# Kernel tuning notes

Measured on AMD Instinct MI355X. Metric: run time of the kernel, lower is better.

The kernel has to match this reference:

```python
import jax, jax.numpy as jnp
import numpy as np

KERNEL_SIZE = 11  # int(resolution / 11.6) with resolution=128
SIGMA = 1.5
K1, K2 = 0.01, 0.03


def gaussian_kernel(k=KERNEL_SIZE, sigma=SIGMA):
    coords = jnp.arange(k, dtype=jnp.float32) - (k - 1) / 2
    g = jnp.exp(-coords ** 2 / (2 * sigma ** 2))
    g = g / g.sum()
    return jnp.outer(g, g)  # (k,k)


def depthwise_conv(x, kern):
    # x: (N,C,H,W), kern: (k,k); depthwise (groups=C), SAME padding, stride 1
    C = x.shape[1]
    k = kern.shape[0]
    w = jnp.broadcast_to(kern[None, None], (C, 1, k, k))
    return jax.lax.conv_general_dilated(
        x, w, window_strides=(1, 1), padding='SAME',
        feature_group_count=C,
        dimension_numbers=('NCHW', 'OIHW', 'NCHW'))


def dssim_map(x, y, kern):
    C1, C2 = K1 ** 2, K2 ** 2
    mu_x = depthwise_conv(x, kern)
    mu_y = depthwise_conv(y, kern)
    sigma_x = depthwise_conv(x * x, kern) - mu_x ** 2
    sigma_y = depthwise_conv(y * y, kern) - mu_y ** 2
    sigma_xy = depthwise_conv(x * y, kern) - mu_x * mu_y
    ssim_num = (2 * mu_x * mu_y + C1) * (2 * sigma_xy + C2)
    ssim_den = (mu_x ** 2 + mu_y ** 2 + C1) * (sigma_x + sigma_y + C2)
    ssim = ssim_num / (ssim_den + 1e-8)
    return (1 - ssim) / 2  # (N,C,H,W)


def poly_mask(pts, H, W):
    # pts: (P,2) polygon vertices (x, y). Vectorized ray-casting point-in-polygon,
    # restricted to the truncated bounding box exactly like the torch code
    # (mask[:, :, ymin:ymax, xmin:xmax] slice), and zeroed if polygon exits frame.
    x, y = pts[:, 0], pts[:, 1]
    xmin, xmax = jnp.floor(x.min()), jnp.floor(x.max())  # == int() for positive coords
    ymin, ymax = jnp.floor(y.min()), jnp.floor(y.max())
    valid = (xmin >= 0) & (ymin >= 0) & (xmax < W) & (ymax < H)
    yy, xx = jnp.meshgrid(jnp.arange(H, dtype=jnp.float32),
                          jnp.arange(W, dtype=jnp.float32), indexing='ij')
    x1, y1 = x[:, None, None], y[:, None, None]        # (P,1,1)
    x2 = jnp.roll(x, -1)[:, None, None]
    y2 = jnp.roll(y, -1)[:, None, None]
    Y, X = yy[None], xx[None]                          # (1,H,W)
    cond = ((y1 > Y) != (y2 > Y)) & (X < (x2 - x1) * (Y - y1) / (y2 - y1 + 1e-6) + x1)
    inside = (cond.sum(axis=0) % 2) == 1               # XOR-fold over edges, (H,W)
    bbox = (yy >= ymin) & (yy < ymax) & (xx >= xmin) & (xx < xmax)
    return jnp.where(valid, (inside & bbox).astype(jnp.float32), 0.0)


def weight_map(lmrk, H, W):
    # lmrk: (68,2). weight = 1 + 3*eyeL + 3*eyeR + 2*mouth (additive, as in torch)
    return (1.0
            + 3.0 * poly_mask(lmrk[36:42], H, W)
            + 3.0 * poly_mask(lmrk[42:48], H, W)
            + 2.0 * poly_mask(lmrk[48:60], H, W))  # (H,W)


def setup_inputs() -> dict:
    key = jax.random.key(0)
    k1, k2, k3 = jax.random.split(key, 3)
    N, C, H, W = 48, 3, 256, 256
    pred = jax.random.normal(k1, (N, C, H, W), dtype=jnp.float32)
    target = jax.random.normal(k2, (N, C, H, W), dtype=jnp.float32)
    # landmarks strictly inside the frame so all polygons are rasterized
    landmarks = 20.0 + 216.0 * jax.random.uniform(k3, (N, 68, 2), dtype=jnp.float32)
    return {"pred": pred, "target": target, "landmarks": landmarks}


def reference(pred, target, landmarks):
    N, C, H, W = pred.shape
    kern = gaussian_kernel()
    # per-sample DSSIM (batch-of-1 conv in torch == batched conv here)
    d = dssim_map(pred, target, kern).mean(axis=(1, 2, 3))          # (N,)
    abs_diff = jnp.abs(pred - target)
    l1 = abs_diff.mean(axis=(1, 2, 3))                              # (N,)
    wmap = jax.vmap(lambda lm: weight_map(lm, H, W))(landmarks)     # (N,H,W)
    lw = (wmap[:, None] * abs_diff).mean(axis=(1, 2, 3))            # (N,)
    return (10.0 * d + 10.0 * l1 + 5.0 * lw).mean()
```

## Files before the change

### kernel.cpp

```cpp
#include <hip/hip_runtime.h>
#include <cmath>

#define HW 256
#define NIMG 48
#define NCH 3
#define NPLANE (NIMG * NCH)
#define STRIP 37
#define NSTRIP 7
#define NIN (STRIP + 10)
#define CHUNK 22
#define NCHUNK 3
#define NSLOT 64

__global__ void zero_ws_kernel(double* ws) {
    if (threadIdx.x < NSLOT) ws[threadIdx.x] = 0.0;
}

__launch_bounds__(256)
__global__ void fused_kernel(const float* __restrict__ pred,
                             const float* __restrict__ target,
                             const float* __restrict__ lmk,
                             double* __restrict__ ws)
{
    const int plane = blockIdx.x;
    const int n     = plane / 3;
    const int r0    = blockIdx.y * STRIP;
    const int x     = threadIdx.x;

    __shared__ float4 mva[2][HW + 10];
    __shared__ float  mvb[2][HW + 10];
    __shared__ float  sxc[STRIP][24];
    __shared__ int    srowflag[STRIP];
    __shared__ float  slm[48];
    __shared__ float  sbbs[12];
    __shared__ float  svalids[3];
    __shared__ float  red[12];

    float g6[6];
    {
        float gg[11]; float gs = 0.f;
#pragma unroll
        for (int q = 0; q < 11; ++q) {
            float c = (float)q - 5.0f;
            gg[q] = expf(-c * c / 4.5f);
            gs += gg[q];
        }
#pragma unroll
        for (int q = 0; q < 6; ++q) g6[q] = gg[q] / gs;
    }
#define GW(j) g6[(j) < 6 ? (j) : 10 - (j)]

    if (x < 48) slm[x] = lmk[n * 136 + 72 + x];
    if (x < 5) {
        const float4 z4 = make_float4(0.f, 0.f, 0.f, 0.f);
        mva[0][x] = z4; mva[0][261 + x] = z4;
        mva[1][x] = z4; mva[1][261 + x] = z4;
        mvb[0][x] = 0.f; mvb[0][261 + x] = 0.f;
        mvb[1][x] = 0.f; mvb[1][261 + x] = 0.f;
    }
    __syncthreads();

    if (x < 3) {
        const int s0 = (x == 0) ? 0 : (x == 1) ? 6 : 12;
        const int L  = (x == 2) ? 12 : 6;
        float xmn = 3e38f, xmx = -3e38f, ymn = 3e38f, ymx = -3e38f;
        for (int q = 0; q < L; ++q) {
            float px = slm[2 * (s0 + q)], py = slm[2 * (s0 + q) + 1];
            xmn = fminf(xmn, px); xmx = fmaxf(xmx, px);
            ymn = fminf(ymn, py); ymx = fmaxf(ymx, py);
        }
        xmn = floorf(xmn); xmx = floorf(xmx); ymn = floorf(ymn); ymx = floorf(ymx);
        sbbs[4 * x + 0] = xmn; sbbs[4 * x + 1] = xmx;
        sbbs[4 * x + 2] = ymn; sbbs[4 * x + 3] = ymx;
        svalids[x] = (xmn >= 0.f && ymn >= 0.f && xmx < 256.f && ymx < 256.f) ? 1.f : 0.f;
    }

#pragma unroll
    for (int u = 0; u < (STRIP * 24 + 255) / 256; ++u) {
        int idx = x + 256 * u;
        if (idx < STRIP * 24) {
            int r = idx / 24, e = idx - r * 24;
            float Y = (float)(r0 + r);
            const int s0 = (e < 6) ? 0 : (e < 12) ? 6 : 12;
            const int L  = (e < 12) ? 6 : 12;
            int il = e - s0;
            int i2 = (il + 1 == L) ? 0 : il + 1;
            float x1 = slm[2 * (s0 + il)], y1 = slm[2 * (s0 + il) + 1];
            float x2 = slm[2 * (s0 + i2)], y2 = slm[2 * (s0 + i2) + 1];
            bool crossing = (y1 > Y) != (y2 > Y);
            float xc = (x2 - x1) * (Y - y1) / (y2 - y1 + 1e-6f) + x1;
            sxc[r][e] = crossing ? xc : -3e38f;
        }
    }
    __syncthreads();

    if (x < STRIP) {
        float Y = (float)(r0 + x);
        int f = 0;
        if (svalids[0] != 0.f && Y >= sbbs[2]  && Y < sbbs[3])  f |= 1;
        if (svalids[1] != 0.f && Y >= sbbs[6]  && Y < sbbs[7])  f |= 2;
        if (svalids[2] != 0.f && Y >= sbbs[10] && Y < sbbs[11]) f |= 4;
        srowflag[x] = f;
    }
    __syncthreads();

    const float* __restrict__ pp = pred   + (size_t)plane * (HW * HW) + x;
    const float* __restrict__ tp = target + (size_t)plane * (HW * HW) + x;

    float rp[11], rt[11];
    float pfap, pfat, pfbp, pfbt;
    {
        int ra = r0 - 5;
        bool va = (ra >= 0);
        pfap = va ? pp[(size_t)ra * HW] : 0.f;
        pfat = va ? tp[(size_t)ra * HW] : 0.f;
        int rb = r0 - 4;
        bool vb = (rb >= 0);
        pfbp = vb ? pp[(size_t)rb * HW] : 0.f;
        pfbt = vb ? tp[(size_t)rb * HW] : 0.f;
    }

    float acc = 0.f, accl1 = 0.f, acclw = 0.f;
    const float X = (float)x;

    for (int c = 0; c < NCHUNK; ++c) {
#pragma unroll
        for (int t = 0; t < CHUNK; ++t) {
            const int i  = CHUNK * c + t;
            const int sr = t % 11;

            if (i < NIN) {
                if ((t & 1) == 0) { rp[sr] = pfap; rt[sr] = pfat; }
                else              { rp[sr] = pfbp; rt[sr] = pfbt; }
                {
                    int rin2 = r0 - 3 + i;
                    bool v = (i + 2 < NIN) && (rin2 >= 0) && (rin2 < HW);
                    float lp = 0.f, lt = 0.f;
                    if (v) {
                        lp = pp[(size_t)rin2 * HW];
                        lt = tp[(size_t)rin2 * HW];
                    }
                    if ((t & 1) == 0) { pfap = lp; pfat = lt; }
                    else              { pfbp = lp; pfbt = lt; }
                }

                if (i >= 5 && i < 5 + STRIP) {
                    int r_in = r0 - 5 + i;
                    if (r_in < HW) {
                        float ad = fabsf(rp[sr] - rt[sr]);
                        accl1 += ad;
                        float wgt = 1.f;
                        const int flags = srowflag[i - 5];
                        if (flags) {
                            const float* xc = sxc[i - 5];
                            int c0 = 0, c1 = 0, c2 = 0;
#pragma unroll
                            for (int e = 0; e < 6; ++e)   c0 += (X < xc[e]) ? 1 : 0;
#pragma unroll
                            for (int e = 6; e < 12; ++e)  c1 += (X < xc[e]) ? 1 : 0;
#pragma unroll
                            for (int e = 12; e < 24; ++e) c2 += (X < xc[e]) ? 1 : 0;
                            if ((flags & 1) && (c0 & 1) && X >= sbbs[0] && X < sbbs[1]) wgt += 3.f;
                            if ((flags & 2) && (c1 & 1) && X >= sbbs[4] && X < sbbs[5]) wgt += 3.f;
                            if ((flags & 4) && (c2 & 1) && X >= sbbs[8] && X < sbbs[9]) wgt += 2.f;
                        }
                        acclw += wgt * ad;
                    }
                }
            }

            if (i >= 10 && i < 10 + STRIP) {
                int r = r0 + i - 10;
                if (r < HW) {
                    float mux = 0.f, muy = 0.f, exx = 0.f, eyy = 0.f, exy = 0.f;
#pragma unroll
                    for (int j = 0; j < 11; ++j) {
                        const int s = (t + 1 + j) % 11;
                        float w = GW(j);
                        float p = rp[s], q = rt[s];
                        float wp = w * p, wt = w * q;
                        mux += wp; muy += wt;
                        exx = fmaf(wp, p, exx);
                        eyy = fmaf(wt, q, eyy);
                        exy = fmaf(wp, q, exy);
                    }
                    mva[t & 1][x + 5] = make_float4(mux, muy, exx, eyy);
                    mvb[t & 1][x + 5] = exy;
                }
            }

            if (i >= 11 && i < 11 + STRIP) {
                int rr = r0 + i - 11;
                if (rr < HW) {
                    const int b = (t + 1) & 1;
                    float Mx = 0.f, My = 0.f, Exx = 0.f, Eyy = 0.f, Exy = 0.f;
#pragma unroll
                    for (int k = 0; k < 11; ++k) {
                        float w = GW(k);
                        float4 m4 = mva[b][x + k];
                        float  m1 = mvb[b][x + k];
                        Mx  = fmaf(w, m4.x, Mx);
                        My  = fmaf(w, m4.y, My);
                        Exx = fmaf(w, m4.z, Exx);
                        Eyy = fmaf(w, m4.w, Eyy);
                        Exy = fmaf(w, m1,  Exy);
                    }
                    float sx  = Exx - Mx * Mx;
                    float sy  = Eyy - My * My;
                    float sxy = Exy - Mx * My;
                    const float C1 = 1e-4f, C2 = 9e-4f;
                    float num = (2.f * Mx * My + C1) * (2.f * sxy + C2);
                    float den = (Mx * Mx + My * My + C1) * (sx + sy + C2);
                    acc += 0.5f * (1.f - num / (den + 1e-8f));
                }
            }

            asm volatile("s_waitcnt lgkmcnt(0)" ::: "memory");
            __builtin_amdgcn_s_barrier();
        }
    }

#pragma unroll
    for (int off = 32; off > 0; off >>= 1) {
        acc   += __shfl_down(acc, off, 64);
        accl1 += __shfl_down(accl1, off, 64);
        acclw += __shfl_down(acclw, off, 64);
    }
    if ((x & 63) == 0) {
        int w = x >> 6;
        red[w] = acc; red[4 + w] = accl1; red[8 + w] = acclw;
    }
    __syncthreads();
    if (x == 0) {
        double s = 10.0 * ((double)red[0] + red[1] + red[2]  + red[3])
                 + 10.0 * ((double)red[4] + red[5] + red[6]  + red[7])
                 +  5.0 * ((double)red[8] + red[9] + red[10] + red[11]);
        atomicAdd(&ws[(blockIdx.y * NPLANE + blockIdx.x) & (NSLOT - 1)], s);
    }
}

__global__ void final_kernel(const double* __restrict__ ws, float* __restrict__ out) {
    double v = ws[threadIdx.x];
#pragma unroll
    for (int off = 32; off > 0; off >>= 1)
        v += __shfl_down(v, off, 64);
    if (threadIdx.x == 0) {
        const double denom = (double)NIMG * NCH * HW * HW;
        out[0] = (float)(v / denom);
    }
}

extern "C" void kernel_launch(void* const* d_in, const int* in_sizes, int n_in,
                              void* d_out, int out_size, void* d_ws, size_t ws_size,
                              hipStream_t stream)
{
    const float* pred   = (const float*)d_in[0];
    const float* target = (const float*)d_in[1];
    const float* lmk    = (const float*)d_in[2];
    float* out  = (float*)d_out;
    double* ws  = (double*)d_ws;

    hipLaunchKernelGGL(zero_ws_kernel, dim3(1), dim3(64), 0, stream, ws);
    hipLaunchKernelGGL(fused_kernel, dim3(NPLANE, NSTRIP), dim3(256), 0, stream,
                       pred, target, lmk, ws);
    hipLaunchKernelGGL(final_kernel, dim3(1), dim3(64), 0, stream, ws, out);
}
```

Measured before the change: 153.0 us.

## Process two rows per barrier phase with double-buffered pairs of vertical sums

Restructures the row-streaming loop so each barrier-separated phase handles two input rows. Vertical convolution results go into paired, double-buffered shared-memory slots, and the horizontal pass reads the previous phase's pair. This roughly halves the number of workgroup barriers per strip and gives more independent work between them. The cost is doubled LDS for the intermediate buffers, a one-row-longer pipeline delay for the horizontal stage, and possibly higher register pressure.

```diff
diff --git a/kernel.cpp b/kernel.cpp
--- a/kernel.cpp
+++ b/kernel.cpp
@@ -8,8 +8,8 @@
 #define STRIP 37
 #define NSTRIP 7
 #define NIN (STRIP + 10)
-#define CHUNK 22
 #define NCHUNK 3
+#define PHASES 25
 #define NSLOT 64
 
 __global__ void zero_ws_kernel(double* ws) {
@@ -27,8 +27,8 @@
     const int r0    = blockIdx.y * STRIP;
     const int x     = threadIdx.x;
 
-    __shared__ float4 mva[2][HW + 10];
-    __shared__ float  mvb[2][HW + 10];
+    __shared__ float4 mva[2][2][HW + 10];
+    __shared__ float  mvb[2][2][HW + 10];
     __shared__ float  sxc[STRIP][24];
     __shared__ int    srowflag[STRIP];
     __shared__ float  slm[48];
@@ -53,10 +53,13 @@
     if (x < 48) slm[x] = lmk[n * 136 + 72 + x];
     if (x < 5) {
         const float4 z4 = make_float4(0.f, 0.f, 0.f, 0.f);
-        mva[0][x] = z4; mva[0][261 + x] = z4;
-        mva[1][x] = z4; mva[1][261 + x] = z4;
-        mvb[0][x] = 0.f; mvb[0][261 + x] = 0.f;
-        mvb[1][x] = 0.f; mvb[1][261 + x] = 0.f;
+#pragma unroll
+        for (int b = 0; b < 2; ++b)
+#pragma unroll
+            for (int q = 0; q < 2; ++q) {
+                mva[b][q][x] = z4; mva[b][q][261 + x] = z4;
+                mvb[b][q][x] = 0.f; mvb[b][q][261 + x] = 0.f;
+            }
     }
     __syncthreads();
 
@@ -125,93 +128,109 @@
 
     for (int c = 0; c < NCHUNK; ++c) {
 #pragma unroll
-        for (int t = 0; t < CHUNK; ++t) {
-            const int i  = CHUNK * c + t;
-            const int sr = t % 11;
-
-            if (i < NIN) {
-                if ((t & 1) == 0) { rp[sr] = pfap; rt[sr] = pfat; }
-                else              { rp[sr] = pfbp; rt[sr] = pfbt; }
-                {
-                    int rin2 = r0 - 3 + i;
-                    bool v = (i + 2 < NIN) && (rin2 >= 0) && (rin2 < HW);
-                    float lp = 0.f, lt = 0.f;
-                    if (v) {
-                        lp = pp[(size_t)rin2 * HW];
-                        lt = tp[(size_t)rin2 * HW];
-                    }
-                    if ((t & 1) == 0) { pfap = lp; pfat = lt; }
-                    else              { pfbp = lp; pfbt = lt; }
+        for (int u = 0; u < 11; ++u) {
+            const int g  = 11 * c + u;
+            if (g >= PHASES) continue;
+            const int i0 = 2 * g;
+            const int wb = g & 1;
+            const int rbuf = wb ^ 1;
+            const int s0 = (2 * u) % 11;
+            const int s1 = (2 * u + 1) % 11;
+
+#pragma unroll
+            for (int q = 0; q < 2; ++q) {
+                const int i  = i0 + q;
+                const int sr = q ? s1 : s0;
+                if (i < NIN) {
+                    if (q == 0) { rp[sr] = pfap; rt[sr] = pfat; }
+                    else        { rp[sr] = pfbp; rt[sr] = pfbt; }
+                    {
+                        int rin2 = r0 - 3 + i;
+                        bool v = (i + 2 < NIN) && (rin2 >= 0) && (rin2 < HW);
+                        float lp = 0.f, lt = 0.f;
+                        if (v) {
+                            lp = pp[(size_t)rin2 * HW];
+                            lt = tp[(size_t)rin2 * HW];
+                        }
+                        if (q == 0) { pfap = lp; pfat = lt; }
+                        else        { pfbp = lp; pfbt = lt; }
+                    }
+                    if (i >= 5 && i < 5 + STRIP) {
+                        int r_in = r0 - 5 + i;
+                        if (r_in < HW) {
+                            float ad = fabsf(rp[sr] - rt[sr]);
+                            accl1 += ad;
+                            float wgt = 1.f;
+                            const int flags = srowflag[i - 5];
+                            if (flags) {
+                                const float* xc = sxc[i - 5];
+                                int c0 = 0, c1 = 0, c2 = 0;
+#pragma unroll
+                                for (int e = 0; e < 6; ++e)   c0 += (X < xc[e]) ? 1 : 0;
+#pragma unroll
+                                for (int e = 6; e < 12; ++e)  c1 += (X < xc[e]) ? 1 : 0;
+#pragma unroll
+                                for (int e = 12; e < 24; ++e) c2 += (X < xc[e]) ? 1 : 0;
+                                if ((flags & 1) && (c0 & 1) && X >= sbbs[0] && X < sbbs[1]) wgt += 3.f;
+                                if ((flags & 2) && (c1 & 1) && X >= sbbs[4] && X < sbbs[5]) wgt += 3.f;
+                                if ((flags & 4) && (c2 & 1) && X >= sbbs[8] && X < sbbs[9]) wgt += 2.f;
+                            }
+                            acclw += wgt * ad;
+                        }
+                    }
                 }
-
-                if (i >= 5 && i < 5 + STRIP) {
-                    int r_in = r0 - 5 + i;
-                    if (r_in < HW) {
-                        float ad = fabsf(rp[sr] - rt[sr]);
-                        accl1 += ad;
-                        float wgt = 1.f;
-                        const int flags = srowflag[i - 5];
-                        if (flags) {
-                            const float* xc = sxc[i - 5];
-                            int c0 = 0, c1 = 0, c2 = 0;
-#pragma unroll
-                            for (int e = 0; e < 6; ++e)   c0 += (X < xc[e]) ? 1 : 0;
-#pragma unroll
-                            for (int e = 6; e < 12; ++e)  c1 += (X < xc[e]) ? 1 : 0;
-#pragma unroll
-                            for (int e = 12; e < 24; ++e) c2 += (X < xc[e]) ? 1 : 0;
-                            if ((flags & 1) && (c0 & 1) && X >= sbbs[0] && X < sbbs[1]) wgt += 3.f;
-                            if ((flags & 2) && (c1 & 1) && X >= sbbs[4] && X < sbbs[5]) wgt += 3.f;
-                            if ((flags & 4) && (c2 & 1) && X >= sbbs[8] && X < sbbs[9]) wgt += 2.f;
-                        }
-                        acclw += wgt * ad;
+            }
+
+#pragma unroll
+            for (int q = 0; q < 2; ++q) {
+                const int i = i0 + q;
+                if (i >= 10 && i < 10 + STRIP) {
+                    int r = r0 + i - 10;
+                    if (r < HW) {
+                        float mux = 0.f, muy = 0.f, exx = 0.f, eyy = 0.f, exy = 0.f;
+#pragma unroll
+                        for (int j = 0; j < 11; ++j) {
+                            const int s = (2 * u + q + 1 + j) % 11;
+                            float w = GW(j);
+                            float p = rp[s], t = rt[s];
+                            float wp = w * p, wt = w * t;
+                            mux += wp; muy += wt;
+                            exx = fmaf(wp, p, exx);
+                            eyy = fmaf(wt, t, eyy);
+                            exy = fmaf(wp, t, exy);
+                        }
+                        mva[wb][q][x + 5] = make_float4(mux, muy, exx, eyy);
+                        mvb[wb][q][x + 5] = exy;
                     }
                 }
             }
 
-            if (i >= 10 && i < 10 + STRIP) {
-                int r = r0 + i - 10;
-                if (r < HW) {
-                    float mux = 0.f, muy = 0.f, exx = 0.f, eyy = 0.f, exy = 0.f;
-#pragma unroll
-                    for (int j = 0; j < 11; ++j) {
-                        const int s = (t + 1 + j) % 11;
-                        float w = GW(j);
-                        float p = rp[s], q = rt[s];
-                        float wp = w * p, wt = w * q;
-                        mux += wp; muy += wt;
-                        exx = fmaf(wp, p, exx);
-                        eyy = fmaf(wt, q, eyy);
-                        exy = fmaf(wp, q, exy);
-                    }
-                    mva[t & 1][x + 5] = make_float4(mux, muy, exx, eyy);
-                    mvb[t & 1][x + 5] = exy;
-                }
-            }
-
-            if (i >= 11 && i < 11 + STRIP) {
-                int rr = r0 + i - 11;
-                if (rr < HW) {
-                    const int b = (t + 1) & 1;
-                    float Mx = 0.f, My = 0.f, Exx = 0.f, Eyy = 0.f, Exy = 0.f;
-#pragma unroll
-                    for (int k = 0; k < 11; ++k) {
-                        float w = GW(k);
-                        float4 m4 = mva[b][x + k];
-                        float  m1 = mvb[b][x + k];
-                        Mx  = fmaf(w, m4.x, Mx);
-                        My  = fmaf(w, m4.y, My);
-                        Exx = fmaf(w, m4.z, Exx);
-                        Eyy = fmaf(w, m4.w, Eyy);
-                        Exy = fmaf(w, m1,  Exy);
-                    }
-                    float sx  = Exx - Mx * Mx;
-                    float sy  = Eyy - My * My;
-                    float sxy = Exy - Mx * My;
-                    const float C1 = 1e-4f, C2 = 9e-4f;
-                    float num = (2.f * Mx * My + C1) * (2.f * sxy + C2);
-                    float den = (Mx * Mx + My * My + C1) * (sx + sy + C2);
-                    acc += 0.5f * (1.f - num / (den + 1e-8f));
+#pragma unroll
+            for (int q = 0; q < 2; ++q) {
+                const int hr = i0 - 12 + q;
+                if (i0 >= 12 - q && hr < STRIP) {
+                    int rr = r0 + hr;
+                    if (rr < HW) {
+                        float Mx = 0.f, My = 0.f, Exx = 0.f, Eyy = 0.f, Exy = 0.f;
+#pragma unroll
+                        for (int k = 0; k < 11; ++k) {
+                            float w = GW(k);
+                            float4 m4 = mva[rbuf][q][x + k];
+                            float  m1 = mvb[rbuf][q][x + k];
+                            Mx  = fmaf(w, m4.x, Mx);
+                            My  = fmaf(w, m4.y, My);
+                            Exx = fmaf(w, m4.z, Exx);
+                            Eyy = fmaf(w, m4.w, Eyy);
+                            Exy = fmaf(w, m1,  Exy);
+                        }
+                        float sx  = Exx - Mx * Mx;
+                        float sy  = Eyy - My * My;
+                        float sxy = Exy - Mx * My;
+                        const float C1 = 1e-4f, C2 = 9e-4f;
+                        float num = (2.f * Mx * My + C1) * (2.f * sxy + C2);
+                        float den = (Mx * Mx + My * My + C1) * (sx + sy + C2);
+                        acc += 0.5f * (1.f - num / (den + 1e-8f));
+                    }
                 }
             }
 
```

New measurement: 179.5 us. 17.3% more time.
